# Kernel optimization log

Measured on AMD Instinct MI355X. Metric: run time of the kernel, lower is better.

## Reference

```python
import jax, jax.numpy as jnp
import numpy as np

TEMPERATURE = 0.07
EPS = 1e-12  # F.normalize eps


def setup_inputs() -> dict:
    key = jax.random.key(0)
    k1, k2 = jax.random.split(key)
    B, D = 4096, 1024
    return {
        "features_1": jax.random.normal(k1, (B, D), dtype=jnp.float32),
        "features_2": jax.random.normal(k2, (B, D), dtype=jnp.float32),
    }


def _l2_normalize(x):
    n = jnp.sqrt(jnp.sum(x * x, axis=1, keepdims=True))
    return x / jnp.maximum(n, EPS)


def reference(features_1, features_2):
    B = features_1.shape[0]
    f1 = _l2_normalize(features_1)
    f2 = _l2_normalize(features_2)
    f = jnp.concatenate([f1, f2], axis=0)  # [2B, D]
    # cosine sim of already-normalized vectors == plain matmul
    sim = (f @ f.T) / TEMPERATURE  # [2B, 2B]
    # denominator: logsumexp over each row excluding the diagonal (self-sim)
    eye = jnp.eye(2 * B, dtype=bool)
    lse = jax.nn.logsumexp(jnp.where(eye, -jnp.inf, sim), axis=1)  # [2B]
    # positives: cross-view pairs (i+B, i) then (i, i+B)
    idx = jnp.arange(B)
    pos = jnp.concatenate([sim[idx + B, idx], sim[idx, idx + B]], axis=0)  # [2B]
    loss = -jnp.mean(pos - lse)
    return loss
```

## Files before the change

kernel.cpp:

```cpp
#include <hip/hip_runtime.h>
#include <hip/hip_bf16.h>
#include <math.h>

#define INV_T (1.0f / 0.07f)

typedef __bf16 bf16x8 __attribute__((ext_vector_type(8)));
typedef float f32x4 __attribute__((ext_vector_type(4)));

__device__ __forceinline__ void gld16(const void* g, void* l) {
    __builtin_amdgcn_global_load_lds(
        (const __attribute__((address_space(1))) unsigned int*)g,
        (__attribute__((address_space(3))) unsigned int*)l,
        16, 0, 0);
}

__global__ __launch_bounds__(256) void norm_kernel(
    const float4* __restrict__ f1, const float4* __restrict__ f2,
    ushort4* __restrict__ F, float* __restrict__ S, float* __restrict__ P,
    int* __restrict__ cnt, int B) {
    const int i = blockIdx.x;
    const int t = threadIdx.x;

    float4 x = f1[i * 256 + t];
    float4 y = f2[i * 256 + t];

    float s1 = x.x * x.x + x.y * x.y + x.z * x.z + x.w * x.w;
    float s2 = y.x * y.x + y.y * y.y + y.z * y.z + y.w * y.w;
    float dd = x.x * y.x + x.y * y.y + x.z * y.z + x.w * y.w;

    for (int o = 32; o > 0; o >>= 1) {
        s1 += __shfl_down(s1, o);
        s2 += __shfl_down(s2, o);
        dd += __shfl_down(dd, o);
    }
    __shared__ float red[4][3];
    const int wv = t >> 6, ln = t & 63;
    if (ln == 0) { red[wv][0] = s1; red[wv][1] = s2; red[wv][2] = dd; }
    __syncthreads();
    s1 = red[0][0] + red[1][0] + red[2][0] + red[3][0];
    s2 = red[0][1] + red[1][1] + red[2][1] + red[3][1];
    dd = red[0][2] + red[1][2] + red[2][2] + red[3][2];

    const float rn1 = 1.0f / fmaxf(sqrtf(s1), 1e-12f);
    const float rn2 = 1.0f / fmaxf(sqrtf(s2), 1e-12f);

    union { ushort4 u; __hip_bfloat16 h[4]; } p;
    p.h[0] = __float2bfloat16(x.x * rn1);
    p.h[1] = __float2bfloat16(x.y * rn1);
    p.h[2] = __float2bfloat16(x.z * rn1);
    p.h[3] = __float2bfloat16(x.w * rn1);
    F[(size_t)i * 256 + t] = p.u;
    p.h[0] = __float2bfloat16(y.x * rn2);
    p.h[1] = __float2bfloat16(y.y * rn2);
    p.h[2] = __float2bfloat16(y.z * rn2);
    p.h[3] = __float2bfloat16(y.w * rn2);
    F[(size_t)(B + i) * 256 + t] = p.u;

    if (t == 0) {
        P[i] = dd * rn1 * rn2;
        S[i] = 0.0f;
        S[B + i] = 0.0f;
        if (i == 0) *cnt = 0;
    }
}

__global__ __launch_bounds__(256, 2) void sim_kernel(
    const __hip_bfloat16* __restrict__ F, float* __restrict__ S,
    const float* __restrict__ P, float* __restrict__ out,
    int* __restrict__ cnt, int N, int B, int D) {
    __shared__ __align__(16) __hip_bfloat16 As[128][64];
    __shared__ __align__(16) __hip_bfloat16 Bs[256][64];

    const int k = blockIdx.x;
    int tj = (int)((sqrtf(4.0f * (float)k + 1.0f) - 1.0f) * 0.5f);
    while ((tj + 1) * (tj + 2) <= k) ++tj;
    while (tj * (tj + 1) > k) --tj;
    const int ti = k - tj * (tj + 1);
    const int bRow = ti * 128;
    const int bCol = tj * 256;

    const int tid  = threadIdx.x;
    const int wave = tid >> 6;
    const int lane = tid & 63;
    const int quad = lane >> 4;
    const int l16  = lane & 15;

    const int srow   = lane >> 3;
    const int ldsOff = (lane & 7) * 8;
    const int srcOff = ((lane & 7) ^ srow) * 8;

    const int waveRow = (wave >> 1) * 64;
    const int waveCol = (wave & 1) * 128;
    const int swz = l16 & 7;

    f32x4 acc[4][8];
#pragma unroll
    for (int mi = 0; mi < 4; ++mi)
#pragma unroll
        for (int ni = 0; ni < 8; ++ni)
            acc[mi][ni] = (f32x4){0.0f, 0.0f, 0.0f, 0.0f};

    for (int kb = 0; kb < D; kb += 64) {
#pragma unroll
        for (int p = 0; p < 4; ++p) {
            const int rowT = (p * 4 + wave) * 8 + srow;
            gld16(&F[(size_t)(bRow + rowT) * D + kb + srcOff], &As[rowT][ldsOff]);
        }
#pragma unroll
        for (int p = 0; p < 8; ++p) {
            const int rowT = (p * 4 + wave) * 8 + srow;
            gld16(&F[(size_t)(bCol + rowT) * D + kb + srcOff], &Bs[rowT][ldsOff]);
        }
        __syncthreads();

#pragma unroll
        for (int ks = 0; ks < 2; ++ks) {
            const int slot = ((ks * 4 + quad) ^ swz) * 8;
            bf16x8 bf[8];
#pragma unroll
            for (int ni = 0; ni < 8; ++ni)
                bf[ni] = *(const bf16x8*)&Bs[waveCol + ni * 16 + l16][slot];
#pragma unroll
            for (int mi = 0; mi < 4; ++mi) {
                const bf16x8 af = *(const bf16x8*)&As[waveRow + mi * 16 + l16][slot];
#pragma unroll
                for (int ni = 0; ni < 8; ++ni)
                    acc[mi][ni] = __builtin_amdgcn_mfma_f32_16x16x32_bf16(
                        af, bf[ni], acc[mi][ni], 0, 0, 0);
            }
        }
        __syncthreads();
    }

#pragma unroll
    for (int mi = 0; mi < 4; ++mi)
#pragma unroll
        for (int ni = 0; ni < 8; ++ni)
#pragma unroll
            for (int r = 0; r < 4; ++r) {
                const int gRow = bRow + waveRow + mi * 16 + quad * 4 + r;
                const int gCol = bCol + waveCol + ni * 16 + l16;
                acc[mi][ni][r] = (gRow < gCol)
                    ? __expf((acc[mi][ni][r] - 1.0f) * INV_T) : 0.0f;
            }

#pragma unroll
    for (int mi = 0; mi < 4; ++mi)
#pragma unroll
        for (int r = 0; r < 4; ++r) {
            const int gRow = bRow + waveRow + mi * 16 + quad * 4 + r;
            float v = 0.0f;
#pragma unroll
            for (int ni = 0; ni < 8; ++ni) v += acc[mi][ni][r];
            v += __shfl_xor(v, 1);
            v += __shfl_xor(v, 2);
            v += __shfl_xor(v, 4);
            v += __shfl_xor(v, 8);
            if (l16 == 0) atomicAdd(&S[gRow], v);
        }

#pragma unroll
    for (int ni = 0; ni < 8; ++ni) {
        float cv = 0.0f;
#pragma unroll
        for (int mi = 0; mi < 4; ++mi)
#pragma unroll
            for (int r = 0; r < 4; ++r) cv += acc[mi][ni][r];
        cv += __shfl_xor(cv, 16);
        cv += __shfl_xor(cv, 32);
        if (quad == 0) atomicAdd(&S[bCol + waveCol + ni * 16 + l16], cv);
    }

    asm volatile("s_waitcnt vmcnt(0) lgkmcnt(0)" ::: "memory");
    __shared__ int lastFlag;
    if (tid == 0) lastFlag = (atomicAdd(cnt, 1) == (int)gridDim.x - 1);
    __syncthreads();
    if (!lastFlag) return;

    float s = 0.0f;
    for (int i = tid; i < N; i += 256) s += __logf(atomicAdd(&S[i], 0.0f));
    float pp = 0.0f;
    for (int i = tid; i < B; i += 256) pp += P[i];
    for (int o = 32; o > 0; o >>= 1) {
        s += __shfl_down(s, o);
        pp += __shfl_down(pp, o);
    }
    __shared__ float redf[4][2];
    if (lane == 0) { redf[wave][0] = s; redf[wave][1] = pp; }
    __syncthreads();
    if (tid == 0) {
        const float sl = redf[0][0] + redf[1][0] + redf[2][0] + redf[3][0];
        const float ps = redf[0][1] + redf[1][1] + redf[2][1] + redf[3][1];
        out[0] = INV_T + sl / (float)N - ps * (2.0f * INV_T / (float)N);
    }
}

extern "C" void kernel_launch(void* const* d_in, const int* in_sizes, int n_in,
                              void* d_out, int out_size, void* d_ws, size_t ws_size,
                              hipStream_t stream) {
    const int D = 1024;
    const int B = in_sizes[0] / D;
    const int N = 2 * B;
    const int M2 = N / 256;
    const int ntiles = M2 * M2 + M2;

    const float* f1 = (const float*)d_in[0];
    const float* f2 = (const float*)d_in[1];

    __hip_bfloat16* F = (__hip_bfloat16*)d_ws;
    float* S = (float*)((char*)d_ws + (size_t)N * D * sizeof(__hip_bfloat16));
    float* P = S + N;
    int* cnt = (int*)(P + B);

    norm_kernel<<<dim3(B), dim3(256), 0, stream>>>(
        (const float4*)f1, (const float4*)f2, (ushort4*)F, S, P, cnt, B);
    sim_kernel<<<dim3(ntiles), dim3(256), 0, stream>>>(
        F, S, P, (float*)d_out, cnt, N, B, D);
}
```

Before: 181.2 us.

## Fuse normalize and similarity into one persistent cooperative kernel with grid sync

Replaces the two launches with a single cooperative persistent kernel. It normalizes rows in a grid-stride loop, calls grid sync, then pulls similarity tiles from an atomic work counter, and after a second grid sync block 0 computes the final reduction. This removes one launch and the last-block atomic detection, and aims to balance load across the triangular tile set. In exchange it adds the cost of grid-wide barriers, and raising occupancy to 3 blocks per CU may constrain registers for the 128-float accumulator. The original two-kernel path remains as a fallback if the cooperative launch fails.

```diff
diff --git a/kernel.cpp b/kernel.cpp
--- a/kernel.cpp
+++ b/kernel.cpp
@@ -1,4 +1,5 @@
 #include <hip/hip_runtime.h>
+#include <hip/hip_cooperative_groups.h>
 #include <hip/hip_bf16.h>
 #include <math.h>
 
@@ -6,12 +7,213 @@
 
 typedef __bf16 bf16x8 __attribute__((ext_vector_type(8)));
 typedef float f32x4 __attribute__((ext_vector_type(4)));
+
+namespace cg = cooperative_groups;
 
 __device__ __forceinline__ void gld16(const void* g, void* l) {
     __builtin_amdgcn_global_load_lds(
         (const __attribute__((address_space(1))) unsigned int*)g,
         (__attribute__((address_space(3))) unsigned int*)l,
         16, 0, 0);
+}
+
+__device__ __forceinline__ float agent_load(const float* p) {
+    return __hip_atomic_load(p, __ATOMIC_RELAXED, __HIP_MEMORY_SCOPE_AGENT);
+}
+
+__global__ __launch_bounds__(256, 3) void fused_kernel(
+    const float4* __restrict__ f1, const float4* __restrict__ f2,
+    ushort4* __restrict__ Fv, float* __restrict__ S, float* __restrict__ P,
+    float* __restrict__ out, int* __restrict__ cnt,
+    int B, int N, int D, int ntiles) {
+    __shared__ __align__(16) __hip_bfloat16 As[128][64];
+    __shared__ __align__(16) __hip_bfloat16 Bs[256][64];
+    __shared__ float red[4][3];
+    __shared__ float redf[4][2];
+    __shared__ int kShared;
+
+    const int tid  = threadIdx.x;
+    const int wave = tid >> 6;
+    const int lane = tid & 63;
+
+    for (int i = blockIdx.x; i < B; i += gridDim.x) {
+        float4 x = f1[i * 256 + tid];
+        float4 y = f2[i * 256 + tid];
+
+        float s1 = x.x * x.x + x.y * x.y + x.z * x.z + x.w * x.w;
+        float s2 = y.x * y.x + y.y * y.y + y.z * y.z + y.w * y.w;
+        float dd = x.x * y.x + x.y * y.y + x.z * y.z + x.w * y.w;
+
+        for (int o = 32; o > 0; o >>= 1) {
+            s1 += __shfl_down(s1, o);
+            s2 += __shfl_down(s2, o);
+            dd += __shfl_down(dd, o);
+        }
+        if (lane == 0) { red[wave][0] = s1; red[wave][1] = s2; red[wave][2] = dd; }
+        __syncthreads();
+        s1 = red[0][0] + red[1][0] + red[2][0] + red[3][0];
+        s2 = red[0][1] + red[1][1] + red[2][1] + red[3][1];
+        dd = red[0][2] + red[1][2] + red[2][2] + red[3][2];
+
+        const float rn1 = 1.0f / fmaxf(sqrtf(s1), 1e-12f);
+        const float rn2 = 1.0f / fmaxf(sqrtf(s2), 1e-12f);
+
+        union { ushort4 u; __hip_bfloat16 h[4]; } p;
+        p.h[0] = __float2bfloat16(x.x * rn1);
+        p.h[1] = __float2bfloat16(x.y * rn1);
+        p.h[2] = __float2bfloat16(x.z * rn1);
+        p.h[3] = __float2bfloat16(x.w * rn1);
+        Fv[(size_t)i * 256 + tid] = p.u;
+        p.h[0] = __float2bfloat16(y.x * rn2);
+        p.h[1] = __float2bfloat16(y.y * rn2);
+        p.h[2] = __float2bfloat16(y.z * rn2);
+        p.h[3] = __float2bfloat16(y.w * rn2);
+        Fv[(size_t)(B + i) * 256 + tid] = p.u;
+
+        if (tid == 0) {
+            P[i] = dd * rn1 * rn2;
+            S[i] = 0.0f;
+            S[B + i] = 0.0f;
+        }
+        __syncthreads();
+    }
+    if (blockIdx.x == 0 && tid == 0) *cnt = 0;
+    cg::this_grid().sync();
+
+    const __hip_bfloat16* __restrict__ F = (const __hip_bfloat16*)Fv;
+
+    const int quad = lane >> 4;
+    const int l16  = lane & 15;
+    const int srow   = lane >> 3;
+    const int ldsOff = (lane & 7) * 8;
+    const int srcOff = ((lane & 7) ^ srow) * 8;
+    const int waveRow = (wave >> 1) * 64;
+    const int waveCol = (wave & 1) * 128;
+    const int swz = l16 & 7;
+
+    for (;;) {
+        if (tid == 0) kShared = atomicAdd(cnt, 1);
+        __syncthreads();
+        const int k = kShared;
+        if (k >= ntiles) break;
+
+        int tj = (int)((sqrtf(4.0f * (float)k + 1.0f) - 1.0f) * 0.5f);
+        while ((tj + 1) * (tj + 2) <= k) ++tj;
+        while (tj * (tj + 1) > k) --tj;
+        const int ti = k - tj * (tj + 1);
+        const int bRow = ti * 128;
+        const int bCol = tj * 256;
+
+        f32x4 acc[4][8];
+#pragma unroll
+        for (int mi = 0; mi < 4; ++mi)
+#pragma unroll
+            for (int ni = 0; ni < 8; ++ni)
+                acc[mi][ni] = (f32x4){0.0f, 0.0f, 0.0f, 0.0f};
+
+        for (int kb = 0; kb < D; kb += 64) {
+#pragma unroll
+            for (int p = 0; p < 4; ++p) {
+                const int rowT = (p * 4 + wave) * 8 + srow;
+                gld16(&F[(size_t)(bRow + rowT) * D + kb + srcOff], &As[rowT][ldsOff]);
+            }
+#pragma unroll
+            for (int p = 0; p < 8; ++p) {
+                const int rowT = (p * 4 + wave) * 8 + srow;
+                gld16(&F[(size_t)(bCol + rowT) * D + kb + srcOff], &Bs[rowT][ldsOff]);
+            }
+            __syncthreads();
+
+#pragma unroll
+            for (int ks = 0; ks < 2; ++ks) {
+                const int slot = ((ks * 4 + quad) ^ swz) * 8;
+                bf16x8 bf[8];
+#pragma unroll
+                for (int ni = 0; ni < 8; ++ni)
+                    bf[ni] = *(const bf16x8*)&Bs[waveCol + ni * 16 + l16][slot];
+#pragma unroll
+                for (int mi = 0; mi < 4; ++mi) {
+                    const bf16x8 af = *(const bf16x8*)&As[waveRow + mi * 16 + l16][slot];
+#pragma unroll
+                    for (int ni = 0; ni < 8; ++ni)
+                        acc[mi][ni] = __builtin_amdgcn_mfma_f32_16x16x32_bf16(
+                            af, bf[ni], acc[mi][ni], 0, 0, 0);
+                }
+            }
+            __syncthreads();
+        }
+
+#pragma unroll
+        for (int mi = 0; mi < 4; ++mi)
+#pragma unroll
+            for (int ni = 0; ni < 8; ++ni)
+#pragma unroll
+                for (int r = 0; r < 4; ++r) {
+                    const int gRow = bRow + waveRow + mi * 16 + quad * 4 + r;
+                    const int gCol = bCol + waveCol + ni * 16 + l16;
+                    acc[mi][ni][r] = (gRow < gCol)
+                        ? __expf((acc[mi][ni][r] - 1.0f) * INV_T) : 0.0f;
+                }
+
+#pragma unroll
+        for (int mi = 0; mi < 4; ++mi)
+#pragma unroll
+            for (int r = 0; r < 4; ++r) {
+                const int gRow = bRow + waveRow + mi * 16 + quad * 4 + r;
+                float v = 0.0f;
+#pragma unroll
+                for (int ni = 0; ni < 8; ++ni) v += acc[mi][ni][r];
+                v += __shfl_xor(v, 1);
+                v += __shfl_xor(v, 2);
+                v += __shfl_xor(v, 4);
+                v += __shfl_xor(v, 8);
+                if (l16 == 0) atomicAdd(&S[gRow], v);
+            }
+
+#pragma unroll
+        for (int ni = 0; ni < 8; ++ni) {
+            float cv = 0.0f;
+#pragma unroll
+            for (int mi = 0; mi < 4; ++mi)
+#pragma unroll
+                for (int r = 0; r < 4; ++r) cv += acc[mi][ni][r];
+            cv += __shfl_xor(cv, 16);
+            cv += __shfl_xor(cv, 32);
+            if (quad == 0) atomicAdd(&S[bCol + waveCol + ni * 16 + l16], cv);
+        }
+    }
+
+    cg::this_grid().sync();
+
+    if (blockIdx.x != 0) return;
+
+    float s0 = 0.0f, s1 = 0.0f, s2 = 0.0f, s3 = 0.0f;
+    for (int i = tid; i < N; i += 1024) {
+        const float a = agent_load(&S[i]);
+        const float b = agent_load(&S[i + 256]);
+        const float c = agent_load(&S[i + 512]);
+        const float d = agent_load(&S[i + 768]);
+        s0 += __logf(a); s1 += __logf(b); s2 += __logf(c); s3 += __logf(d);
+    }
+    float s = (s0 + s1) + (s2 + s3);
+
+    float pp = 0.0f;
+    for (int i = tid; i < B; i += 1024) {
+        pp += agent_load(&P[i]) + agent_load(&P[i + 256]) +
+              agent_load(&P[i + 512]) + agent_load(&P[i + 768]);
+    }
+
+    for (int o = 32; o > 0; o >>= 1) {
+        s += __shfl_down(s, o);
+        pp += __shfl_down(pp, o);
+    }
+    if (lane == 0) { redf[wave][0] = s; redf[wave][1] = pp; }
+    __syncthreads();
+    if (tid == 0) {
+        const float sl = redf[0][0] + redf[1][0] + redf[2][0] + redf[3][0];
+        const float ps = redf[0][1] + redf[1][1] + redf[2][1] + redf[3][1];
+        out[0] = INV_T + sl / (float)N - ps * (2.0f * INV_T / (float)N);
+    }
 }
 
 __global__ __launch_bounds__(256) void norm_kernel(
@@ -212,8 +414,47 @@
     float* P = S + N;
     int* cnt = (int*)(P + B);
 
-    norm_kernel<<<dim3(B), dim3(256), 0, stream>>>(
-        (const float4*)f1, (const float4*)f2, (ushort4*)F, S, P, cnt, B);
-    sim_kernel<<<dim3(ntiles), dim3(256), 0, stream>>>(
-        F, S, P, (float*)d_out, cnt, N, B, D);
-}
+    static int coopBlocks = -2;
+    if (coopBlocks == -2) {
+        int maxb = 0;
+        if (hipOccupancyMaxActiveBlocksPerMultiprocessor(
+                &maxb, fused_kernel, 256, 0) == hipSuccess && maxb > 0) {
+            int dev = 0;
+            hipGetDevice(&dev);
+            hipDeviceProp_t prop;
+            int cus = 256;
+            if (hipGetDeviceProperties(&prop, dev) == hipSuccess &&
+                prop.multiProcessorCount > 0)
+                cus = prop.multiProcessorCount;
+            coopBlocks = maxb * cus;
+        } else {
+            coopBlocks = -1;
+        }
+    }
+
+    bool done = false;
+    if (coopBlocks > 0) {
+        const float4* a1 = (const float4*)f1;
+        const float4* a2 = (const float4*)f2;
+        ushort4* Fv = (ushort4*)F;
+        float* Sv = S;
+        float* Pv = P;
+        float* ov = (float*)d_out;
+        int* cv = cnt;
+        int Bi = B, Ni = N, Di = D, nt = ntiles;
+        void* args[] = {&a1, &a2, &Fv, &Sv, &Pv, &ov, &cv, &Bi, &Ni, &Di, &nt};
+        if (hipLaunchCooperativeKernel(fused_kernel, dim3(coopBlocks),
+                                       dim3(256), args, 0, stream) == hipSuccess) {
+            done = true;
+        } else {
+            coopBlocks = -1;
+        }
+    }
+
+    if (!done) {
+        norm_kernel<<<dim3(B), dim3(256), 0, stream>>>(
+            (const float4*)f1, (const float4*)f2, (ushort4*)F, S, P, cnt, B);
+        sim_kernel<<<dim3(ntiles), dim3(256), 0, stream>>>(
+            F, S, P, (float*)d_out, cnt, N, B, D);
+    }
+}
```

New measurement: 490.4 us. +170.6%, slower.
